# Kernel optimization log

Measured on AMD Instinct MI355X. Metric: run time of the kernel, lower is better.

Reference implementation:

```python
import jax, jax.numpy as jnp
import numpy as np
import math

D_MODEL = 256
N_HEADS = 8
NUM_NODES = 20
KSIZE = 3
EPS = 1e-5


def _ln(x, g, b):
    m = jnp.mean(x, axis=-1, keepdims=True)
    v = jnp.mean(jnp.square(x - m), axis=-1, keepdims=True)
    return (x - m) * jax.lax.rsqrt(v + EPS) * g + b


def _conv1d(x_bdn, w_oik):
    # x: [B, D, N], w: [O, I, K], SAME padding, no bias
    return jax.lax.conv_general_dilated(
        x_bdn, w_oik, window_strides=(1,), padding='SAME',
        dimension_numbers=('NCH', 'OIH', 'NCH'))


def setup_inputs() -> dict:
    key = jax.random.key(0)
    ks = jax.random.split(key, 12)
    B, N, D, H, K = 8192, NUM_NODES, D_MODEL, N_HEADS, KSIZE
    s = 1.0 / math.sqrt(D * K)
    inp = {
        'x': jax.random.normal(ks[0], (B, N, D), jnp.float32),
        'wq': jax.random.normal(ks[1], (D, D, K), jnp.float32) * s,
        'wk': jax.random.normal(ks[2], (D, D, K), jnp.float32) * s,
        'wv': jax.random.normal(ks[3], (D, D, K), jnp.float32) * s,
        'gq': jnp.ones((D,), jnp.float32), 'bq': jnp.zeros((D,), jnp.float32),
        'gk': jnp.ones((D,), jnp.float32), 'bk': jnp.zeros((D,), jnp.float32),
        'gv': jnp.ones((D,), jnp.float32), 'bv': jnp.zeros((D,), jnp.float32),
        'rel_table': jax.random.normal(ks[4], (2 * N - 1, H), jnp.float32) * 0.02,
        'gbias': jax.random.normal(ks[5], (H, N, N), jnp.float32) * 0.02,
        'alpha': jnp.float32(1.0),
        'wo': jax.random.normal(ks[6], (D, D), jnp.float32) * (1.0 / math.sqrt(D)),
        'bo': jnp.zeros((D,), jnp.float32),
    }
    return inp


def reference(x, wq, wk, wv, gq, bq, gk, bk, gv, bv, rel_table, gbias, alpha, wo, bo):
    B, N, D = x.shape
    H = N_HEADS
    dk = D // H
    xp = jnp.transpose(x, (0, 2, 1))  # [B, D, N]
    q = x + _ln(jnp.transpose(_conv1d(xp, wq), (0, 2, 1)), gq, bq)
    k = x + _ln(jnp.transpose(_conv1d(xp, wk), (0, 2, 1)), gk, bk)
    v = x + _ln(jnp.transpose(_conv1d(xp, wv), (0, 2, 1)), gv, bv)
    q = q.reshape(B, N, H, dk).transpose(0, 2, 1, 3)  # [B, H, N, dk]
    k = k.reshape(B, N, H, dk).transpose(0, 2, 1, 3)
    v = v.reshape(B, N, H, dk).transpose(0, 2, 1, 3)
    scores = jnp.einsum('bhnd,bhmd->bhnm', q, k) / math.sqrt(dk)
    # relative position bias: index table [2N-1, H] -> [1, H, N, N]
    coords = jnp.arange(N)
    rel_idx = coords[:, None] - coords[None, :] + N - 1  # [N, N]
    rel_bias = rel_table[rel_idx]  # [N, N, H]
    scores = scores + jnp.transpose(rel_bias, (2, 0, 1))[None]
    scores = scores + gbias[None] * alpha
    attn = jax.nn.softmax(scores, axis=-1)
    out = jnp.einsum('bhnm,bhmd->bhnd', attn, v)  # dropout p=0
    out = out.transpose(0, 2, 1, 3).reshape(B, N, D)
    return out @ wo.T + bo
```

## Files before the change

kernel.cpp:

```cpp
#include <hip/hip_runtime.h>
#include <hip/hip_bf16.h>
#include <stdint.h>

#define BATCH 8192
#define NNODE 20
#define MROWS 163840
#define KCONV 768
#define NCONV 768

typedef __bf16 bf16x8 __attribute__((ext_vector_type(8)));
typedef float f32x4 __attribute__((ext_vector_type(4)));
typedef unsigned short u16x4 __attribute__((ext_vector_type(4)));

#define GLOBAL_AS __attribute__((address_space(1)))
#define LDS_AS __attribute__((address_space(3)))

__device__ __forceinline__ void load_lds16(const void* g, void* l) {
  __builtin_amdgcn_global_load_lds((const GLOBAL_AS uint32_t*)g,
                                   (LDS_AS uint32_t*)l, 16, 0, 0);
}

__device__ __forceinline__ float bf2f(unsigned short u) {
  union { unsigned int i; float f; } x;
  x.i = ((unsigned int)u) << 16;
  return x.f;
}

__global__ void prep_kernel(const float* __restrict__ x,
                            const float* __restrict__ wq,
                            const float* __restrict__ wk,
                            const float* __restrict__ wv,
                            const float* __restrict__ wo,
                            __hip_bfloat16* __restrict__ xb,
                            __hip_bfloat16* __restrict__ WcT,
                            __hip_bfloat16* __restrict__ wob,
                            int* __restrict__ zrow) {
  const int stride = gridDim.x * blockDim.x;
  const int gid = blockIdx.x * blockDim.x + threadIdx.x;

  if (gid < 128) zrow[gid] = 0;

  const int n8 = (MROWS * 256) / 8;
  for (int i8 = gid; i8 < n8; i8 += stride) {
    const float4* xp = ((const float4*)x) + (size_t)i8 * 2;
    float4 a = xp[0];
    float4 b = xp[1];
    __align__(16) __hip_bfloat16 h[8];
    h[0] = __float2bfloat16(a.x); h[1] = __float2bfloat16(a.y);
    h[2] = __float2bfloat16(a.z); h[3] = __float2bfloat16(a.w);
    h[4] = __float2bfloat16(b.x); h[5] = __float2bfloat16(b.y);
    h[6] = __float2bfloat16(b.z); h[7] = __float2bfloat16(b.w);
    ((int4*)xb)[i8] = *(const int4*)h;
  }

  for (int idx = gid; idx < NCONV * KCONV; idx += stride) {
    int n = idx / KCONV;
    int j = idx - n * KCONV;
    int c = n >> 8, o = n & 255;
    int t = j >> 8, i = j & 255;
    const float* w = (c == 0) ? wq : (c == 1) ? wk : wv;
    WcT[idx] = __float2bfloat16(w[(o * 256 + i) * 3 + t]);
  }

  for (int idx = gid; idx < 256 * 256; idx += stride) {
    wob[idx] = __float2bfloat16(wo[idx]);
  }
}

__global__ __launch_bounds__(256) void conv_gemm_kernel(
    const __hip_bfloat16* __restrict__ xb,
    const __hip_bfloat16* __restrict__ WcT,
    __hip_bfloat16* __restrict__ y,
    const __hip_bfloat16* __restrict__ zrow) {
  __shared__ __align__(16) __hip_bfloat16 As[128 * 64];
  __shared__ __align__(16) __hip_bfloat16 Bs[128 * 64];

  const int tid = threadIdx.x;
  const int lane = tid & 63;
  const int wave = tid >> 6;
  const int wm = (wave >> 1) << 6;
  const int wn = (wave & 1) << 6;
  const int l16 = lane & 15;
  const int quad = lane >> 4;
  const int m0 = blockIdx.x * 128;
  const int n0 = blockIdx.y * 128;

  const __hip_bfloat16* a_base[4];
  const __hip_bfloat16* z_base[4];
  const __hip_bfloat16* b_base[4];
  int a_node[4];
  int lds_off[4];
#pragma unroll
  for (int it = 0; it < 4; ++it) {
    int flat = ((it * 4 + wave) << 6) + lane;
    int row = flat >> 3;
    int seg = flat & 7;
    int seg_g = seg ^ (row & 7);
    int gr = m0 + row;
    int b = gr / 20;
    int node = gr - b * 20;
    a_node[it] = node;
    a_base[it] = xb + (long)(gr - 1) * 256 + seg_g * 8;
    z_base[it] = zrow + seg_g * 8;
    b_base[it] = WcT + (size_t)(n0 + row) * KCONV + seg_g * 8;
    lds_off[it] = (it * 4 + wave) << 9;
  }

  f32x4 acc[4][4];
  const f32x4 zero = {0.f, 0.f, 0.f, 0.f};
#pragma unroll
  for (int i = 0; i < 4; ++i)
#pragma unroll
    for (int j = 0; j < 4; ++j) acc[i][j] = zero;

  for (int kt = 0; kt < 12; ++kt) {
    const int t = kt >> 2;
    const int i0 = (kt & 3) << 6;
    const int k0 = kt << 6;
#pragma unroll
    for (int it = 0; it < 4; ++it) {
      bool ok = (unsigned)(a_node[it] + t - 1) < 20u;
      const __hip_bfloat16* ga = ok ? (a_base[it] + t * 256 + i0) : z_base[it];
      load_lds16(ga, &As[lds_off[it]]);
      load_lds16(b_base[it] + k0, &Bs[lds_off[it]]);
    }
    __syncthreads();

#pragma unroll
    for (int kk = 0; kk < 64; kk += 32) {
      const int sx = (((kk >> 3) + quad) ^ (l16 & 7)) << 3;
      bf16x8 af[4], bfr[4];
#pragma unroll
      for (int i = 0; i < 4; ++i)
        af[i] = *(const bf16x8*)&As[((wm + i * 16 + l16) << 6) + sx];
#pragma unroll
      for (int j = 0; j < 4; ++j)
        bfr[j] = *(const bf16x8*)&Bs[((wn + j * 16 + l16) << 6) + sx];
#pragma unroll
      for (int i = 0; i < 4; ++i)
#pragma unroll
        for (int j = 0; j < 4; ++j)
          acc[i][j] = __builtin_amdgcn_mfma_f32_16x16x32_bf16(af[i], bfr[j],
                                                              acc[i][j], 0, 0, 0);
    }
    __syncthreads();
  }

#pragma unroll
  for (int i = 0; i < 4; ++i)
#pragma unroll
    for (int j = 0; j < 4; ++j)
#pragma unroll
      for (int r = 0; r < 4; ++r) {
        int row = m0 + wm + i * 16 + quad * 4 + r;
        int col = n0 + wn + j * 16 + l16;
        y[(size_t)row * NCONV + col] = __float2bfloat16(acc[i][j][r]);
      }
}

__global__ void ln_kernel(__hip_bfloat16* __restrict__ y,
                          const __hip_bfloat16* __restrict__ xb,
                          const float* __restrict__ gq, const float* __restrict__ bq,
                          const float* __restrict__ gk, const float* __restrict__ bk,
                          const float* __restrict__ gv, const float* __restrict__ bv) {
  const int lane = threadIdx.x & 63;
  const int wave = threadIdx.x >> 6;
  const int row = blockIdx.x * 4 + wave;
  const int d0 = lane << 2;

  u16x4 yv[3];
#pragma unroll
  for (int c = 0; c < 3; ++c)
    yv[c] = *(const u16x4*)&y[(size_t)row * 768 + c * 256 + d0];
  u16x4 xv = *(const u16x4*)&xb[((size_t)row << 8) + d0];

  float4 g4[3], b4[3];
  g4[0] = *(const float4*)&gq[d0]; b4[0] = *(const float4*)&bq[d0];
  g4[1] = *(const float4*)&gk[d0]; b4[1] = *(const float4*)&bk[d0];
  g4[2] = *(const float4*)&gv[d0]; b4[2] = *(const float4*)&bv[d0];

  float f[3][4];
  float sum[3] = {0.f, 0.f, 0.f}, sq[3] = {0.f, 0.f, 0.f};
#pragma unroll
  for (int c = 0; c < 3; ++c)
#pragma unroll
    for (int s = 0; s < 4; ++s) {
      float v = bf2f(yv[c][s]);
      f[c][s] = v;
      sum[c] += v;
      sq[c] += v * v;
    }
#pragma unroll
  for (int off = 32; off > 0; off >>= 1)
#pragma unroll
    for (int c = 0; c < 3; ++c) {
      sum[c] += __shfl_xor(sum[c], off, 64);
      sq[c] += __shfl_xor(sq[c], off, 64);
    }

  float rx[4];
#pragma unroll
  for (int s = 0; s < 4; ++s) rx[s] = bf2f(xv[s]);

#pragma unroll
  for (int c = 0; c < 3; ++c) {
    float mean = sum[c] * (1.0f / 256.0f);
    float var = sq[c] * (1.0f / 256.0f) - mean * mean;
    float rstd = rsqrtf(var + 1e-5f);
    const float* g = (const float*)&g4[c];
    const float* bb = (const float*)&b4[c];
    __align__(8) __hip_bfloat16 h[4];
#pragma unroll
    for (int s = 0; s < 4; ++s)
      h[s] = __float2bfloat16(rx[s] + (f[c][s] - mean) * rstd * g[s] + bb[s]);
    *(int2*)&y[(size_t)row * 768 + c * 256 + d0] = *(const int2*)h;
  }
}

#define YST 776
__global__ __launch_bounds__(256) void attn2_kernel(
    const __hip_bfloat16* __restrict__ y,
    const float* __restrict__ rel,
    const float* __restrict__ gbias,
    const float* __restrict__ alpha_p,
    __hip_bfloat16* __restrict__ ao) {
  __shared__ __align__(16) __hip_bfloat16 yS[20 * YST];
  __shared__ float scS[8 * 20 * 20];

  const int b = blockIdx.x;
  const int tid = threadIdx.x;
  const float alpha = alpha_p[0];

  const int4* src4 = (const int4*)(y + (size_t)b * NNODE * 768);
#pragma unroll
  for (int p = 0; p < 8; ++p) {
    int idx = tid + p * 256;
    if (idx < 1920) {
      int r = idx / 96;
      int c = idx - r * 96;
      *(int4*)&yS[r * YST + c * 8] = src4[idx];
    }
  }
  __syncthreads();

#pragma unroll
  for (int p = 0; p < 4; ++p) {
    int flat = tid + p * 256;
    if (flat < 800) {
      int h = flat / 100;
      int rem = flat - h * 100;
      int i = rem / 5;
      int j0 = (rem - i * 5) * 4;
      const unsigned short* qp = (const unsigned short*)&yS[i * YST + h * 32];
      float qf[32];
#pragma unroll
      for (int d = 0; d < 32; ++d) qf[d] = bf2f(qp[d]);
      float4 gb4 = *(const float4*)&gbias[h * 400 + i * 20 + j0];
#pragma unroll
      for (int jj = 0; jj < 4; ++jj) {
        int j = j0 + jj;
        const unsigned short* kp = (const unsigned short*)&yS[j * YST + 256 + h * 32];
        float dot = 0.f;
#pragma unroll
        for (int d = 0; d < 32; ++d) dot += qf[d] * bf2f(kp[d]);
        scS[h * 400 + i * 20 + j] = dot * 0.17677669529663687f +
                                    rel[(i - j + 19) * 8 + h] +
                                    ((const float*)&gb4)[jj] * alpha;
      }
    }
  }
  __syncthreads();

  if (tid < 160) {
    float* row = scS + tid * 20;
    float mx = row[0];
#pragma unroll
    for (int j = 1; j < 20; ++j) mx = fmaxf(mx, row[j]);
    float s = 0.f;
    float e[20];
#pragma unroll
    for (int j = 0; j < 20; ++j) {
      e[j] = __expf(row[j] - mx);
      s += e[j];
    }
    float inv = 1.0f / s;
#pragma unroll
    for (int j = 0; j < 20; ++j) row[j] = e[j] * inv;
  }
  __syncthreads();

#pragma unroll
  for (int p = 0; p < 5; ++p) {
    int flat = tid + p * 256;
    int col = flat & 255;
    int i0 = (flat >> 8) << 2;
    int h = col >> 5;
    const unsigned short* vp = (const unsigned short*)yS;
    float o[4] = {0.f, 0.f, 0.f, 0.f};
#pragma unroll
    for (int j = 0; j < 20; ++j) {
      float vv = bf2f(vp[j * YST + 512 + col]);
#pragma unroll
      for (int ii = 0; ii < 4; ++ii)
        o[ii] += scS[h * 400 + (i0 + ii) * 20 + j] * vv;
    }
#pragma unroll
    for (int ii = 0; ii < 4; ++ii)
      ao[(((size_t)(b * NNODE + i0 + ii)) << 8) + col] = __float2bfloat16(o[ii]);
  }
}

__global__ __launch_bounds__(256) void proj_gemm_kernel(
    const __hip_bfloat16* __restrict__ ao,
    const __hip_bfloat16* __restrict__ wob,
    const float* __restrict__ bo,
    float* __restrict__ out) {
  __shared__ __align__(16) __hip_bfloat16 As[128 * 64];
  __shared__ __align__(16) __hip_bfloat16 Bs[128 * 64];

  const int tid = threadIdx.x;
  const int lane = tid & 63;
  const int wave = tid >> 6;
  const int wm = (wave >> 1) << 6;
  const int wn = (wave & 1) << 6;
  const int l16 = lane & 15;
  const int quad = lane >> 4;
  const int m0 = blockIdx.x * 128;
  const int n0 = blockIdx.y * 128;

  const __hip_bfloat16* a_base[4];
  const __hip_bfloat16* b_base[4];
  int lds_off[4];
#pragma unroll
  for (int it = 0; it < 4; ++it) {
    int flat = ((it * 4 + wave) << 6) + lane;
    int row = flat >> 3;
    int seg = flat & 7;
    int seg_g = seg ^ (row & 7);
    a_base[it] = ao + (((size_t)(m0 + row)) << 8) + seg_g * 8;
    b_base[it] = wob + (((size_t)(n0 + row)) << 8) + seg_g * 8;
    lds_off[it] = (it * 4 + wave) << 9;
  }

  f32x4 acc[4][4];
  const f32x4 zero = {0.f, 0.f, 0.f, 0.f};
#pragma unroll
  for (int i = 0; i < 4; ++i)
#pragma unroll
    for (int j = 0; j < 4; ++j) acc[i][j] = zero;

  for (int kt = 0; kt < 4; ++kt) {
    const int k0 = kt << 6;
#pragma unroll
    for (int it = 0; it < 4; ++it) {
      load_lds16(a_base[it] + k0, &As[lds_off[it]]);
      load_lds16(b_base[it] + k0, &Bs[lds_off[it]]);
    }
    __syncthreads();

#pragma unroll
    for (int kk = 0; kk < 64; kk += 32) {
      const int sx = (((kk >> 3) + quad) ^ (l16 & 7)) << 3;
      bf16x8 af[4], bfr[4];
#pragma unroll
      for (int i = 0; i < 4; ++i)
        af[i] = *(const bf16x8*)&As[((wm + i * 16 + l16) << 6) + sx];
#pragma unroll
      for (int j = 0; j < 4; ++j)
        bfr[j] = *(const bf16x8*)&Bs[((wn + j * 16 + l16) << 6) + sx];
#pragma unroll
      for (int i = 0; i < 4; ++i)
#pragma unroll
        for (int j = 0; j < 4; ++j)
          acc[i][j] = __builtin_amdgcn_mfma_f32_16x16x32_bf16(af[i], bfr[j],
                                                              acc[i][j], 0, 0, 0);
    }
    __syncthreads();
  }

#pragma unroll
  for (int i = 0; i < 4; ++i)
#pragma unroll
    for (int j = 0; j < 4; ++j) {
      int col = n0 + wn + j * 16 + l16;
      float bias = bo[col];
#pragma unroll
      for (int r = 0; r < 4; ++r) {
        int row = m0 + wm + i * 16 + quad * 4 + r;
        out[(size_t)row * 256 + col] = acc[i][j][r] + bias;
      }
    }
}

extern "C" void kernel_launch(void* const* d_in, const int* in_sizes, int n_in,
                              void* d_out, int out_size, void* d_ws, size_t ws_size,
                              hipStream_t stream) {
  const float* x     = (const float*)d_in[0];
  const float* wq    = (const float*)d_in[1];
  const float* wk    = (const float*)d_in[2];
  const float* wv    = (const float*)d_in[3];
  const float* gq    = (const float*)d_in[4];
  const float* bq    = (const float*)d_in[5];
  const float* gk    = (const float*)d_in[6];
  const float* bk    = (const float*)d_in[7];
  const float* gv    = (const float*)d_in[8];
  const float* bv    = (const float*)d_in[9];
  const float* rel   = (const float*)d_in[10];
  const float* gbias = (const float*)d_in[11];
  const float* alpha = (const float*)d_in[12];
  const float* wo    = (const float*)d_in[13];
  const float* bo    = (const float*)d_in[14];
  float* out = (float*)d_out;

  char* ws = (char*)d_ws;
  __hip_bfloat16* xb  = (__hip_bfloat16*)(ws);
  __hip_bfloat16* y   = (__hip_bfloat16*)(ws + 83886080);
  __hip_bfloat16* ao  = (__hip_bfloat16*)(ws + 335544320);
  __hip_bfloat16* WcT = (__hip_bfloat16*)(ws + 419430400);
  __hip_bfloat16* wob = (__hip_bfloat16*)(ws + 420610048);
  int*            zr  = (int*)(ws + 420741120);

  prep_kernel<<<8192, 256, 0, stream>>>(x, wq, wk, wv, wo, xb, WcT, wob, zr);
  conv_gemm_kernel<<<dim3(1280, 6), 256, 0, stream>>>(xb, WcT, y,
                                                      (const __hip_bfloat16*)zr);
  ln_kernel<<<40960, 256, 0, stream>>>(y, xb, gq, bq, gk, bk, gv, bv);
  attn2_kernel<<<8192, 256, 0, stream>>>(y, rel, gbias, alpha, ao);
  proj_gemm_kernel<<<dim3(1280, 2), 256, 0, stream>>>(ao, wob, bo, out);
}
```

Before: 865.0 us.

## Fuse LayerNorm into attention kernel and loop N-tiles inside conv GEMM

Removes the standalone LayerNorm+residual kernel and performs the normalization on the y rows already staged in LDS inside the attention kernel, loading x rows alongside. This avoids a full extra read and write pass over the large y intermediate and one kernel launch. The conv GEMM now launches one block per M tile and iterates over all six N tiles, reusing A rows across tiles, at the cost of fewer blocks and less parallelism.

New measurement: 926.0 us. 1.07x slower.

```diff
diff --git a/kernel.cpp b/kernel.cpp
--- a/kernel.cpp
+++ b/kernel.cpp
@@ -10,7 +10,6 @@
 
 typedef __bf16 bf16x8 __attribute__((ext_vector_type(8)));
 typedef float f32x4 __attribute__((ext_vector_type(4)));
-typedef unsigned short u16x4 __attribute__((ext_vector_type(4)));
 
 #define GLOBAL_AS __attribute__((address_space(1)))
 #define LDS_AS __attribute__((address_space(3)))
@@ -83,11 +82,10 @@
   const int l16 = lane & 15;
   const int quad = lane >> 4;
   const int m0 = blockIdx.x * 128;
-  const int n0 = blockIdx.y * 128;
 
   const __hip_bfloat16* a_base[4];
   const __hip_bfloat16* z_base[4];
-  const __hip_bfloat16* b_base[4];
+  size_t b_off[4];
   int a_node[4];
   int lds_off[4];
 #pragma unroll
@@ -102,143 +100,151 @@
     a_node[it] = node;
     a_base[it] = xb + (long)(gr - 1) * 256 + seg_g * 8;
     z_base[it] = zrow + seg_g * 8;
-    b_base[it] = WcT + (size_t)(n0 + row) * KCONV + seg_g * 8;
+    b_off[it] = (size_t)row * KCONV + seg_g * 8;
     lds_off[it] = (it * 4 + wave) << 9;
   }
 
-  f32x4 acc[4][4];
-  const f32x4 zero = {0.f, 0.f, 0.f, 0.f};
-#pragma unroll
-  for (int i = 0; i < 4; ++i)
-#pragma unroll
-    for (int j = 0; j < 4; ++j) acc[i][j] = zero;
-
-  for (int kt = 0; kt < 12; ++kt) {
-    const int t = kt >> 2;
-    const int i0 = (kt & 3) << 6;
-    const int k0 = kt << 6;
-#pragma unroll
-    for (int it = 0; it < 4; ++it) {
-      bool ok = (unsigned)(a_node[it] + t - 1) < 20u;
-      const __hip_bfloat16* ga = ok ? (a_base[it] + t * 256 + i0) : z_base[it];
-      load_lds16(ga, &As[lds_off[it]]);
-      load_lds16(b_base[it] + k0, &Bs[lds_off[it]]);
-    }
-    __syncthreads();
-
-#pragma unroll
-    for (int kk = 0; kk < 64; kk += 32) {
-      const int sx = (((kk >> 3) + quad) ^ (l16 & 7)) << 3;
-      bf16x8 af[4], bfr[4];
-#pragma unroll
-      for (int i = 0; i < 4; ++i)
-        af[i] = *(const bf16x8*)&As[((wm + i * 16 + l16) << 6) + sx];
+  for (int nt = 0; nt < 6; ++nt) {
+    const int n0 = nt << 7;
+    const __hip_bfloat16* bb = WcT + (size_t)n0 * KCONV;
+
+    f32x4 acc[4][4];
+    const f32x4 zero = {0.f, 0.f, 0.f, 0.f};
+#pragma unroll
+    for (int i = 0; i < 4; ++i)
+#pragma unroll
+      for (int j = 0; j < 4; ++j) acc[i][j] = zero;
+
+    for (int kt = 0; kt < 12; ++kt) {
+      const int t = kt >> 2;
+      const int i0 = (kt & 3) << 6;
+      const int k0 = kt << 6;
+#pragma unroll
+      for (int it = 0; it < 4; ++it) {
+        bool ok = (unsigned)(a_node[it] + t - 1) < 20u;
+        const __hip_bfloat16* ga = ok ? (a_base[it] + t * 256 + i0) : z_base[it];
+        load_lds16(ga, &As[lds_off[it]]);
+        load_lds16(bb + b_off[it] + k0, &Bs[lds_off[it]]);
+      }
+      __syncthreads();
+
+#pragma unroll
+      for (int kk = 0; kk < 64; kk += 32) {
+        const int sx = (((kk >> 3) + quad) ^ (l16 & 7)) << 3;
+        bf16x8 af[4], bfr[4];
+#pragma unroll
+        for (int i = 0; i < 4; ++i)
+          af[i] = *(const bf16x8*)&As[((wm + i * 16 + l16) << 6) + sx];
+#pragma unroll
+        for (int j = 0; j < 4; ++j)
+          bfr[j] = *(const bf16x8*)&Bs[((wn + j * 16 + l16) << 6) + sx];
+#pragma unroll
+        for (int i = 0; i < 4; ++i)
+#pragma unroll
+          for (int j = 0; j < 4; ++j)
+            acc[i][j] = __builtin_amdgcn_mfma_f32_16x16x32_bf16(af[i], bfr[j],
+                                                                acc[i][j], 0, 0, 0);
+      }
+      __syncthreads();
+    }
+
+#pragma unroll
+    for (int i = 0; i < 4; ++i)
 #pragma unroll
       for (int j = 0; j < 4; ++j)
-        bfr[j] = *(const bf16x8*)&Bs[((wn + j * 16 + l16) << 6) + sx];
-#pragma unroll
-      for (int i = 0; i < 4; ++i)
-#pragma unroll
-        for (int j = 0; j < 4; ++j)
-          acc[i][j] = __builtin_amdgcn_mfma_f32_16x16x32_bf16(af[i], bfr[j],
-                                                              acc[i][j], 0, 0, 0);
-    }
-    __syncthreads();
-  }
-
-#pragma unroll
-  for (int i = 0; i < 4; ++i)
-#pragma unroll
-    for (int j = 0; j < 4; ++j)
-#pragma unroll
-      for (int r = 0; r < 4; ++r) {
-        int row = m0 + wm + i * 16 + quad * 4 + r;
-        int col = n0 + wn + j * 16 + l16;
-        y[(size_t)row * NCONV + col] = __float2bfloat16(acc[i][j][r]);
-      }
-}
-
-__global__ void ln_kernel(__hip_bfloat16* __restrict__ y,
-                          const __hip_bfloat16* __restrict__ xb,
-                          const float* __restrict__ gq, const float* __restrict__ bq,
-                          const float* __restrict__ gk, const float* __restrict__ bk,
-                          const float* __restrict__ gv, const float* __restrict__ bv) {
-  const int lane = threadIdx.x & 63;
-  const int wave = threadIdx.x >> 6;
-  const int row = blockIdx.x * 4 + wave;
-  const int d0 = lane << 2;
-
-  u16x4 yv[3];
-#pragma unroll
-  for (int c = 0; c < 3; ++c)
-    yv[c] = *(const u16x4*)&y[(size_t)row * 768 + c * 256 + d0];
-  u16x4 xv = *(const u16x4*)&xb[((size_t)row << 8) + d0];
-
-  float4 g4[3], b4[3];
-  g4[0] = *(const float4*)&gq[d0]; b4[0] = *(const float4*)&bq[d0];
-  g4[1] = *(const float4*)&gk[d0]; b4[1] = *(const float4*)&bk[d0];
-  g4[2] = *(const float4*)&gv[d0]; b4[2] = *(const float4*)&bv[d0];
-
-  float f[3][4];
-  float sum[3] = {0.f, 0.f, 0.f}, sq[3] = {0.f, 0.f, 0.f};
-#pragma unroll
-  for (int c = 0; c < 3; ++c)
-#pragma unroll
-    for (int s = 0; s < 4; ++s) {
-      float v = bf2f(yv[c][s]);
-      f[c][s] = v;
-      sum[c] += v;
-      sq[c] += v * v;
-    }
-#pragma unroll
-  for (int off = 32; off > 0; off >>= 1)
-#pragma unroll
-    for (int c = 0; c < 3; ++c) {
-      sum[c] += __shfl_xor(sum[c], off, 64);
-      sq[c] += __shfl_xor(sq[c], off, 64);
-    }
-
-  float rx[4];
-#pragma unroll
-  for (int s = 0; s < 4; ++s) rx[s] = bf2f(xv[s]);
-
-#pragma unroll
-  for (int c = 0; c < 3; ++c) {
-    float mean = sum[c] * (1.0f / 256.0f);
-    float var = sq[c] * (1.0f / 256.0f) - mean * mean;
-    float rstd = rsqrtf(var + 1e-5f);
-    const float* g = (const float*)&g4[c];
-    const float* bb = (const float*)&b4[c];
-    __align__(8) __hip_bfloat16 h[4];
-#pragma unroll
-    for (int s = 0; s < 4; ++s)
-      h[s] = __float2bfloat16(rx[s] + (f[c][s] - mean) * rstd * g[s] + bb[s]);
-    *(int2*)&y[(size_t)row * 768 + c * 256 + d0] = *(const int2*)h;
+#pragma unroll
+        for (int r = 0; r < 4; ++r) {
+          int row = m0 + wm + i * 16 + quad * 4 + r;
+          int col = n0 + wn + j * 16 + l16;
+          y[(size_t)row * NCONV + col] = __float2bfloat16(acc[i][j][r]);
+        }
   }
 }
 
 #define YST 776
 __global__ __launch_bounds__(256) void attn2_kernel(
     const __hip_bfloat16* __restrict__ y,
+    const __hip_bfloat16* __restrict__ xb,
+    const float* __restrict__ gq, const float* __restrict__ bq,
+    const float* __restrict__ gk, const float* __restrict__ bk,
+    const float* __restrict__ gv, const float* __restrict__ bv,
     const float* __restrict__ rel,
     const float* __restrict__ gbias,
     const float* __restrict__ alpha_p,
     __hip_bfloat16* __restrict__ ao) {
   __shared__ __align__(16) __hip_bfloat16 yS[20 * YST];
+  __shared__ __align__(16) __hip_bfloat16 xS[20 * 256];
   __shared__ float scS[8 * 20 * 20];
 
   const int b = blockIdx.x;
   const int tid = threadIdx.x;
   const float alpha = alpha_p[0];
 
-  const int4* src4 = (const int4*)(y + (size_t)b * NNODE * 768);
+  const int4* ysrc = (const int4*)(y + (size_t)b * NNODE * 768);
 #pragma unroll
   for (int p = 0; p < 8; ++p) {
     int idx = tid + p * 256;
     if (idx < 1920) {
       int r = idx / 96;
       int c = idx - r * 96;
-      *(int4*)&yS[r * YST + c * 8] = src4[idx];
+      *(int4*)&yS[r * YST + c * 8] = ysrc[idx];
+    }
+  }
+  const int4* xsrc = (const int4*)(xb + ((size_t)b * NNODE << 8));
+#pragma unroll
+  for (int p = 0; p < 3; ++p) {
+    int idx = tid + p * 256;
+    if (idx < 640) ((int4*)xS)[idx] = xsrc[idx];
+  }
+  __syncthreads();
+
+  if (tid < 240) {
+    const int r = tid >> 2;
+    const int lane4 = tid & 3;
+    const int node = r / 3;
+    const int c = r - node * 3;
+    const int d0 = lane4 << 6;
+    const float* g = (c == 0) ? gq : (c == 1) ? gk : gv;
+    const float* be = (c == 0) ? bq : (c == 1) ? bk : bv;
+    __hip_bfloat16* yrow = &yS[node * YST + (c << 8) + d0];
+    const __hip_bfloat16* xrow = &xS[(node << 8) + d0];
+
+    float sum = 0.f, sq = 0.f;
+#pragma unroll
+    for (int s = 0; s < 8; ++s) {
+      bf16x8 v = *(const bf16x8*)&yrow[s << 3];
+#pragma unroll
+      for (int e = 0; e < 8; ++e) {
+        float f = (float)v[e];
+        sum += f;
+        sq += f * f;
+      }
+    }
+    sum += __shfl_xor(sum, 1, 64); sq += __shfl_xor(sq, 1, 64);
+    sum += __shfl_xor(sum, 2, 64); sq += __shfl_xor(sq, 2, 64);
+    float mean = sum * (1.0f / 256.0f);
+    float var = sq * (1.0f / 256.0f) - mean * mean;
+    float rstd = rsqrtf(var + 1e-5f);
+
+#pragma unroll
+    for (int s = 0; s < 8; ++s) {
+      bf16x8 v = *(const bf16x8*)&yrow[s << 3];
+      bf16x8 xv = *(const bf16x8*)&xrow[s << 3];
+      float4 g0 = *(const float4*)&g[d0 + (s << 3)];
+      float4 g1 = *(const float4*)&g[d0 + (s << 3) + 4];
+      float4 b0 = *(const float4*)&be[d0 + (s << 3)];
+      float4 b1 = *(const float4*)&be[d0 + (s << 3) + 4];
+      const float* gp = (const float*)&g0;
+      const float* gq2 = (const float*)&g1;
+      const float* bp = (const float*)&b0;
+      const float* bq2 = (const float*)&b1;
+      __align__(16) __hip_bfloat16 h[8];
+#pragma unroll
+      for (int e = 0; e < 4; ++e) {
+        h[e] = __float2bfloat16((float)xv[e] + ((float)v[e] - mean) * rstd * gp[e] + bp[e]);
+        h[e + 4] = __float2bfloat16((float)xv[e + 4] + ((float)v[e + 4] - mean) * rstd * gq2[e] + bq2[e]);
+      }
+      *(int4*)&yrow[s << 3] = *(const int4*)h;
     }
   }
   __syncthreads();
@@ -421,9 +427,9 @@
   int*            zr  = (int*)(ws + 420741120);
 
   prep_kernel<<<8192, 256, 0, stream>>>(x, wq, wk, wv, wo, xb, WcT, wob, zr);
-  conv_gemm_kernel<<<dim3(1280, 6), 256, 0, stream>>>(xb, WcT, y,
-                                                      (const __hip_bfloat16*)zr);
-  ln_kernel<<<40960, 256, 0, stream>>>(y, xb, gq, bq, gk, bk, gv, bv);
-  attn2_kernel<<<8192, 256, 0, stream>>>(y, rel, gbias, alpha, ao);
+  conv_gemm_kernel<<<1280, 256, 0, stream>>>(xb, WcT, y,
+                                             (const __hip_bfloat16*)zr);
+  attn2_kernel<<<8192, 256, 0, stream>>>(y, xb, gq, bq, gk, bk, gv, bv,
+                                         rel, gbias, alpha, ao);
   proj_gemm_kernel<<<dim3(1280, 2), 256, 0, stream>>>(ao, wob, bo, out);
 }
```
